# Kernel optimization log

Hardware: AMD Instinct MI355X
Metric: run time of the kernel (lower is better)

Reference implementation:

```python
import jax, jax.numpy as jnp
import numpy as np

N = 50000
E = 800000
D = 64


def sage_conv(x, src, dst, Wl, Wr, b, n_nodes):
    # message = x[src]; mean-aggregate by dst; then lin_l(mean) + lin_r(x) + b
    msg = x[src]                                             # [E, D] gather
    ssum = jax.ops.segment_sum(msg, dst, num_segments=n_nodes)  # [N, D]
    cnt = jax.ops.segment_sum(jnp.ones((msg.shape[0],), dtype=x.dtype), dst,
                              num_segments=n_nodes)          # [N]
    mean = ssum / jnp.maximum(cnt, 1.0)[:, None]             # scatter-mean (empty rows -> 0)
    return mean @ Wl.T + x @ Wr.T + b


def setup_inputs() -> dict:
    key = jax.random.key(0)
    ks = jax.random.split(key, 8)
    scale = 1.0 / np.sqrt(D)
    x = jax.random.normal(ks[0], (N, D), dtype=jnp.float32)
    edge_index = jax.random.randint(ks[1], (2, E), 0, N, dtype=jnp.int64)
    Wl1 = jax.random.normal(ks[2], (D, D), dtype=jnp.float32) * scale
    Wr1 = jax.random.normal(ks[3], (D, D), dtype=jnp.float32) * scale
    b1 = jnp.zeros((D,), dtype=jnp.float32)
    Wl2 = jax.random.normal(ks[4], (D, D), dtype=jnp.float32) * scale
    Wr2 = jax.random.normal(ks[5], (D, D), dtype=jnp.float32) * scale
    b2 = jnp.zeros((D,), dtype=jnp.float32)
    return {"x": x, "edge_index": edge_index, "Wl1": Wl1, "Wr1": Wr1, "b1": b1,
            "Wl2": Wl2, "Wr2": Wr2, "b2": b2}


def reference(x, edge_index, Wl1, Wr1, b1, Wl2, Wr2, b2):
    src, dst = edge_index[0], edge_index[1]
    n = x.shape[0]
    h = sage_conv(x, src, dst, Wl1, Wr1, b1, n)
    h = jax.nn.relu(h)
    out = sage_conv(h, src, dst, Wl2, Wr2, b2, n)
    return out
```

## Files before the change

### kernel.cpp

```cpp
#include <hip/hip_runtime.h>

#define D 64
#define CAP 64
#define LPAD 132
#define NPART 8

__global__ void fill_kernel(const int* __restrict__ src, const int* __restrict__ dst,
                            int* __restrict__ cnti, int* __restrict__ eidx,
                            int E, int N) {
    int part = blockIdx.x & (NPART - 1);
    int bip  = blockIdx.x >> 3;
    int span = (N + NPART - 1) / NPART;
    int lo = part * span;
    int hi = lo + span; if (hi > N) hi = N;
    int i = bip * blockDim.x + threadIdx.x;
    int stride = (gridDim.x >> 3) * blockDim.x;
    for (; i < E; i += stride) {
        int t = dst[i];
        if (t >= lo && t < hi) {
            int pos = atomicAdd(&cnti[t], 1);
            if (pos < CAP) eidx[(size_t)t * CAP + pos] = src[i];
        }
    }
}

__device__ __forceinline__ float dot4acc(float4 a, float4 w, float c) {
    c = fmaf(a.x, w.x, c);
    c = fmaf(a.y, w.y, c);
    c = fmaf(a.z, w.z, c);
    c = fmaf(a.w, w.w, c);
    return c;
}

__global__ __launch_bounds__(256, 2) void fused_kernel(
                             const float* __restrict__ xin,
                             const int* __restrict__ eidx,
                             const int* __restrict__ cnti,
                             const float* __restrict__ Wl,
                             const float* __restrict__ Wr,
                             const float* __restrict__ bias,
                             float* __restrict__ out,
                             int do_relu, int N) {
    __shared__ float ain[64][LPAD];
    __shared__ float wsh[64][LPAD];
    __shared__ float bsh[64];
    int tid = threadIdx.x;
    int nb = blockIdx.x * 64;

    for (int c = tid; c < 64 * 32; c += 256) {
        int d = c >> 5, kc = c & 31;
        float4 v;
        if (kc < 16) v = *reinterpret_cast<const float4*>(Wl + d * D + kc * 4);
        else         v = *reinterpret_cast<const float4*>(Wr + d * D + (kc - 16) * 4);
        *reinterpret_cast<float4*>(&wsh[d][kc * 4]) = v;
    }
    if (tid < 64) bsh[tid] = bias[tid];

    int g = tid >> 4;
    int lane = tid & 15;
    for (int ni = 0; ni < 4; ++ni) {
        int ln = ni * 16 + g;
        int node = nb + ln; if (node >= N) node = N - 1;
        int deg = cnti[node];
        int lim = deg > CAP ? CAP : deg;
        int last = lim - 1;
        const int* ep = eidx + (size_t)node * CAP;
        float4 acc = make_float4(0.f, 0.f, 0.f, 0.f);
        for (int i = 0; i < lim; i += 8) {
            int j1 = i + 1 > last ? last : i + 1;
            int j2 = i + 2 > last ? last : i + 2;
            int j3 = i + 3 > last ? last : i + 3;
            int j4 = i + 4 > last ? last : i + 4;
            int j5 = i + 5 > last ? last : i + 5;
            int j6 = i + 6 > last ? last : i + 6;
            int j7 = i + 7 > last ? last : i + 7;
            int e0 = ep[i];  int e1 = ep[j1]; int e2 = ep[j2]; int e3 = ep[j3];
            int e4 = ep[j4]; int e5 = ep[j5]; int e6 = ep[j6]; int e7 = ep[j7];
            float4 v0 = *reinterpret_cast<const float4*>(xin + (size_t)e0 * D + lane * 4);
            float4 v1 = *reinterpret_cast<const float4*>(xin + (size_t)e1 * D + lane * 4);
            float4 v2 = *reinterpret_cast<const float4*>(xin + (size_t)e2 * D + lane * 4);
            float4 v3 = *reinterpret_cast<const float4*>(xin + (size_t)e3 * D + lane * 4);
            float4 v4 = *reinterpret_cast<const float4*>(xin + (size_t)e4 * D + lane * 4);
            float4 v5 = *reinterpret_cast<const float4*>(xin + (size_t)e5 * D + lane * 4);
            float4 v6 = *reinterpret_cast<const float4*>(xin + (size_t)e6 * D + lane * 4);
            float4 v7 = *reinterpret_cast<const float4*>(xin + (size_t)e7 * D + lane * 4);
            float m1 = (i + 1 <= last) ? 1.f : 0.f;
            float m2 = (i + 2 <= last) ? 1.f : 0.f;
            float m3 = (i + 3 <= last) ? 1.f : 0.f;
            float m4 = (i + 4 <= last) ? 1.f : 0.f;
            float m5 = (i + 5 <= last) ? 1.f : 0.f;
            float m6 = (i + 6 <= last) ? 1.f : 0.f;
            float m7 = (i + 7 <= last) ? 1.f : 0.f;
            acc.x += v0.x; acc.y += v0.y; acc.z += v0.z; acc.w += v0.w;
            acc.x = fmaf(v1.x, m1, acc.x); acc.y = fmaf(v1.y, m1, acc.y);
            acc.z = fmaf(v1.z, m1, acc.z); acc.w = fmaf(v1.w, m1, acc.w);
            acc.x = fmaf(v2.x, m2, acc.x); acc.y = fmaf(v2.y, m2, acc.y);
            acc.z = fmaf(v2.z, m2, acc.z); acc.w = fmaf(v2.w, m2, acc.w);
            acc.x = fmaf(v3.x, m3, acc.x); acc.y = fmaf(v3.y, m3, acc.y);
            acc.z = fmaf(v3.z, m3, acc.z); acc.w = fmaf(v3.w, m3, acc.w);
            acc.x = fmaf(v4.x, m4, acc.x); acc.y = fmaf(v4.y, m4, acc.y);
            acc.z = fmaf(v4.z, m4, acc.z); acc.w = fmaf(v4.w, m4, acc.w);
            acc.x = fmaf(v5.x, m5, acc.x); acc.y = fmaf(v5.y, m5, acc.y);
            acc.z = fmaf(v5.z, m5, acc.z); acc.w = fmaf(v5.w, m5, acc.w);
            acc.x = fmaf(v6.x, m6, acc.x); acc.y = fmaf(v6.y, m6, acc.y);
            acc.z = fmaf(v6.z, m6, acc.z); acc.w = fmaf(v6.w, m6, acc.w);
            acc.x = fmaf(v7.x, m7, acc.x); acc.y = fmaf(v7.y, m7, acc.y);
            acc.z = fmaf(v7.z, m7, acc.z); acc.w = fmaf(v7.w, m7, acc.w);
        }
        float r = 1.0f / fmaxf((float)deg, 1.0f);
        acc.x *= r; acc.y *= r; acc.z *= r; acc.w *= r;
        *reinterpret_cast<float4*>(&ain[ln][lane * 4]) = acc;
        float4 xv = *reinterpret_cast<const float4*>(xin + (size_t)node * D + lane * 4);
        *reinterpret_cast<float4*>(&ain[ln][64 + lane * 4]) = xv;
    }
    __syncthreads();

    int tx = tid & 15;
    int ty = tid >> 4;

    float4 acc0 = make_float4(0.f, 0.f, 0.f, 0.f);
    float4 acc1 = make_float4(0.f, 0.f, 0.f, 0.f);
    float4 acc2 = make_float4(0.f, 0.f, 0.f, 0.f);
    float4 acc3 = make_float4(0.f, 0.f, 0.f, 0.f);

#pragma unroll 2
    for (int kc = 0; kc < 32; ++kc) {
        float4 a0 = *reinterpret_cast<const float4*>(&ain[ty +  0][kc * 4]);
        float4 a1 = *reinterpret_cast<const float4*>(&ain[ty + 16][kc * 4]);
        float4 a2 = *reinterpret_cast<const float4*>(&ain[ty + 32][kc * 4]);
        float4 a3 = *reinterpret_cast<const float4*>(&ain[ty + 48][kc * 4]);
        float4 w0 = *reinterpret_cast<const float4*>(&wsh[tx +  0][kc * 4]);
        float4 w1 = *reinterpret_cast<const float4*>(&wsh[tx + 16][kc * 4]);
        float4 w2 = *reinterpret_cast<const float4*>(&wsh[tx + 32][kc * 4]);
        float4 w3 = *reinterpret_cast<const float4*>(&wsh[tx + 48][kc * 4]);
        acc0.x = dot4acc(a0, w0, acc0.x); acc0.y = dot4acc(a0, w1, acc0.y);
        acc0.z = dot4acc(a0, w2, acc0.z); acc0.w = dot4acc(a0, w3, acc0.w);
        acc1.x = dot4acc(a1, w0, acc1.x); acc1.y = dot4acc(a1, w1, acc1.y);
        acc1.z = dot4acc(a1, w2, acc1.z); acc1.w = dot4acc(a1, w3, acc1.w);
        acc2.x = dot4acc(a2, w0, acc2.x); acc2.y = dot4acc(a2, w1, acc2.y);
        acc2.z = dot4acc(a2, w2, acc2.z); acc2.w = dot4acc(a2, w3, acc2.w);
        acc3.x = dot4acc(a3, w0, acc3.x); acc3.y = dot4acc(a3, w1, acc3.y);
        acc3.z = dot4acc(a3, w2, acc3.z); acc3.w = dot4acc(a3, w3, acc3.w);
    }

    float b0 = bsh[tx], b1 = bsh[tx + 16], b2 = bsh[tx + 32], b3 = bsh[tx + 48];
#define STORE_ROW(ACCV, I)                                                    \
    {                                                                         \
        int node = nb + ty + 16 * (I);                                        \
        if (node < N) {                                                       \
            float v0 = ACCV.x + b0, v1 = ACCV.y + b1,                         \
                  v2 = ACCV.z + b2, v3 = ACCV.w + b3;                         \
            if (do_relu) {                                                    \
                v0 = fmaxf(v0, 0.f); v1 = fmaxf(v1, 0.f);                     \
                v2 = fmaxf(v2, 0.f); v3 = fmaxf(v3, 0.f);                     \
            }                                                                 \
            float* op = out + (size_t)node * D;                               \
            op[tx] = v0; op[tx + 16] = v1; op[tx + 32] = v2; op[tx + 48] = v3;\
        }                                                                     \
    }
    STORE_ROW(acc0, 0)
    STORE_ROW(acc1, 1)
    STORE_ROW(acc2, 2)
    STORE_ROW(acc3, 3)
#undef STORE_ROW
}

extern "C" void kernel_launch(void* const* d_in, const int* in_sizes, int n_in,
                              void* d_out, int out_size, void* d_ws, size_t ws_size,
                              hipStream_t stream) {
    const float* x   = (const float*)d_in[0];
    const int*   ei  = (const int*)d_in[1];
    const float* Wl1 = (const float*)d_in[2];
    const float* Wr1 = (const float*)d_in[3];
    const float* b1  = (const float*)d_in[4];
    const float* Wl2 = (const float*)d_in[5];
    const float* Wr2 = (const float*)d_in[6];
    const float* b2  = (const float*)d_in[7];

    int N_ = in_sizes[0] / D;
    int E_ = in_sizes[1] / 2;
    const int* src = ei;
    const int* dst = ei + E_;

    int*   cnti = (int*)d_ws;
    int*   eidx = cnti + N_;
    float* h    = (float*)(eidx + (size_t)N_ * CAP);
    float* outp = (float*)d_out;

    hipMemsetAsync(cnti, 0, (size_t)N_ * sizeof(int), stream);
    fill_kernel<<<2048, 256, 0, stream>>>(src, dst, cnti, eidx, E_, N_);

    int blocks = (N_ + 63) / 64;
    fused_kernel<<<blocks, 256, 0, stream>>>(x, eidx, cnti, Wl1, Wr1, b1, h, 1, N_);
    fused_kernel<<<blocks, 256, 0, stream>>>(h, eidx, cnti, Wl2, Wr2, b2, outp, 0, N_);
}
```

Baseline: 219.4 us.

## Gather neighbor features from bf16 copies and store weights as bf16 in LDS

Adds a conversion kernel that writes a bf16 copy of x, and makes layer 1 also emit a bf16 copy of h. The neighbor gather in the fused kernel now reads 8 bytes per lane instead of 16, which halves the random-access gather traffic. Weights are packed as bf16 in LDS so the kernel uses less shared memory, and launch bounds are raised to 3 blocks per SM. The cost is an extra conversion pass, extra bf16 stores, and reduced precision in the aggregation and weights, which may break a tight tolerance.

```diff
diff --git a/kernel.cpp b/kernel.cpp
--- a/kernel.cpp
+++ b/kernel.cpp
@@ -3,7 +3,28 @@
 #define D 64
 #define CAP 64
 #define LPAD 132
+#define WPAD 136
 #define NPART 8
+
+__device__ __forceinline__ unsigned int f2bf(float f) {
+    unsigned int u = __float_as_uint(f);
+    return (u + 0x7fffu + ((u >> 16) & 1u)) >> 16;
+}
+__device__ __forceinline__ float bflo(unsigned int u) { return __uint_as_float(u << 16); }
+__device__ __forceinline__ float bfhi(unsigned int u) { return __uint_as_float(u & 0xffff0000u); }
+
+__global__ void convert_kernel(const float* __restrict__ in,
+                               unsigned short* __restrict__ outh, int total4) {
+    int i = blockIdx.x * blockDim.x + threadIdx.x;
+    int stride = gridDim.x * blockDim.x;
+    for (; i < total4; i += stride) {
+        float4 v = *reinterpret_cast<const float4*>(in + (size_t)i * 4);
+        uint2 p;
+        p.x = f2bf(v.x) | (f2bf(v.y) << 16);
+        p.y = f2bf(v.z) | (f2bf(v.w) << 16);
+        *reinterpret_cast<uint2*>(outh + (size_t)i * 4) = p;
+    }
+}
 
 __global__ void fill_kernel(const int* __restrict__ src, const int* __restrict__ dst,
                             int* __restrict__ cnti, int* __restrict__ eidx,
@@ -32,17 +53,19 @@
     return c;
 }
 
-__global__ __launch_bounds__(256, 2) void fused_kernel(
+__global__ __launch_bounds__(256, 3) void fused_kernel(
                              const float* __restrict__ xin,
+                             const unsigned short* __restrict__ gath,
                              const int* __restrict__ eidx,
                              const int* __restrict__ cnti,
                              const float* __restrict__ Wl,
                              const float* __restrict__ Wr,
                              const float* __restrict__ bias,
                              float* __restrict__ out,
+                             unsigned short* __restrict__ outh,
                              int do_relu, int N) {
     __shared__ float ain[64][LPAD];
-    __shared__ float wsh[64][LPAD];
+    __shared__ unsigned short wsh[64][WPAD];
     __shared__ float bsh[64];
     int tid = threadIdx.x;
     int nb = blockIdx.x * 64;
@@ -52,7 +75,10 @@
         float4 v;
         if (kc < 16) v = *reinterpret_cast<const float4*>(Wl + d * D + kc * 4);
         else         v = *reinterpret_cast<const float4*>(Wr + d * D + (kc - 16) * 4);
-        *reinterpret_cast<float4*>(&wsh[d][kc * 4]) = v;
+        uint2 p;
+        p.x = f2bf(v.x) | (f2bf(v.y) << 16);
+        p.y = f2bf(v.z) | (f2bf(v.w) << 16);
+        *reinterpret_cast<uint2*>(&wsh[d][kc * 4]) = p;
     }
     if (tid < 64) bsh[tid] = bias[tid];
 
@@ -76,14 +102,14 @@
             int j7 = i + 7 > last ? last : i + 7;
             int e0 = ep[i];  int e1 = ep[j1]; int e2 = ep[j2]; int e3 = ep[j3];
             int e4 = ep[j4]; int e5 = ep[j5]; int e6 = ep[j6]; int e7 = ep[j7];
-            float4 v0 = *reinterpret_cast<const float4*>(xin + (size_t)e0 * D + lane * 4);
-            float4 v1 = *reinterpret_cast<const float4*>(xin + (size_t)e1 * D + lane * 4);
-            float4 v2 = *reinterpret_cast<const float4*>(xin + (size_t)e2 * D + lane * 4);
-            float4 v3 = *reinterpret_cast<const float4*>(xin + (size_t)e3 * D + lane * 4);
-            float4 v4 = *reinterpret_cast<const float4*>(xin + (size_t)e4 * D + lane * 4);
-            float4 v5 = *reinterpret_cast<const float4*>(xin + (size_t)e5 * D + lane * 4);
-            float4 v6 = *reinterpret_cast<const float4*>(xin + (size_t)e6 * D + lane * 4);
-            float4 v7 = *reinterpret_cast<const float4*>(xin + (size_t)e7 * D + lane * 4);
+            uint2 w0 = *reinterpret_cast<const uint2*>(gath + (size_t)e0 * D + lane * 4);
+            uint2 w1 = *reinterpret_cast<const uint2*>(gath + (size_t)e1 * D + lane * 4);
+            uint2 w2 = *reinterpret_cast<const uint2*>(gath + (size_t)e2 * D + lane * 4);
+            uint2 w3 = *reinterpret_cast<const uint2*>(gath + (size_t)e3 * D + lane * 4);
+            uint2 w4 = *reinterpret_cast<const uint2*>(gath + (size_t)e4 * D + lane * 4);
+            uint2 w5 = *reinterpret_cast<const uint2*>(gath + (size_t)e5 * D + lane * 4);
+            uint2 w6 = *reinterpret_cast<const uint2*>(gath + (size_t)e6 * D + lane * 4);
+            uint2 w7 = *reinterpret_cast<const uint2*>(gath + (size_t)e7 * D + lane * 4);
             float m1 = (i + 1 <= last) ? 1.f : 0.f;
             float m2 = (i + 2 <= last) ? 1.f : 0.f;
             float m3 = (i + 3 <= last) ? 1.f : 0.f;
@@ -91,21 +117,22 @@
             float m5 = (i + 5 <= last) ? 1.f : 0.f;
             float m6 = (i + 6 <= last) ? 1.f : 0.f;
             float m7 = (i + 7 <= last) ? 1.f : 0.f;
-            acc.x += v0.x; acc.y += v0.y; acc.z += v0.z; acc.w += v0.w;
-            acc.x = fmaf(v1.x, m1, acc.x); acc.y = fmaf(v1.y, m1, acc.y);
-            acc.z = fmaf(v1.z, m1, acc.z); acc.w = fmaf(v1.w, m1, acc.w);
-            acc.x = fmaf(v2.x, m2, acc.x); acc.y = fmaf(v2.y, m2, acc.y);
-            acc.z = fmaf(v2.z, m2, acc.z); acc.w = fmaf(v2.w, m2, acc.w);
-            acc.x = fmaf(v3.x, m3, acc.x); acc.y = fmaf(v3.y, m3, acc.y);
-            acc.z = fmaf(v3.z, m3, acc.z); acc.w = fmaf(v3.w, m3, acc.w);
-            acc.x = fmaf(v4.x, m4, acc.x); acc.y = fmaf(v4.y, m4, acc.y);
-            acc.z = fmaf(v4.z, m4, acc.z); acc.w = fmaf(v4.w, m4, acc.w);
-            acc.x = fmaf(v5.x, m5, acc.x); acc.y = fmaf(v5.y, m5, acc.y);
-            acc.z = fmaf(v5.z, m5, acc.z); acc.w = fmaf(v5.w, m5, acc.w);
-            acc.x = fmaf(v6.x, m6, acc.x); acc.y = fmaf(v6.y, m6, acc.y);
-            acc.z = fmaf(v6.z, m6, acc.z); acc.w = fmaf(v6.w, m6, acc.w);
-            acc.x = fmaf(v7.x, m7, acc.x); acc.y = fmaf(v7.y, m7, acc.y);
-            acc.z = fmaf(v7.z, m7, acc.z); acc.w = fmaf(v7.w, m7, acc.w);
+            acc.x += bflo(w0.x); acc.y += bfhi(w0.x);
+            acc.z += bflo(w0.y); acc.w += bfhi(w0.y);
+            acc.x = fmaf(bflo(w1.x), m1, acc.x); acc.y = fmaf(bfhi(w1.x), m1, acc.y);
+            acc.z = fmaf(bflo(w1.y), m1, acc.z); acc.w = fmaf(bfhi(w1.y), m1, acc.w);
+            acc.x = fmaf(bflo(w2.x), m2, acc.x); acc.y = fmaf(bfhi(w2.x), m2, acc.y);
+            acc.z = fmaf(bflo(w2.y), m2, acc.z); acc.w = fmaf(bfhi(w2.y), m2, acc.w);
+            acc.x = fmaf(bflo(w3.x), m3, acc.x); acc.y = fmaf(bfhi(w3.x), m3, acc.y);
+            acc.z = fmaf(bflo(w3.y), m3, acc.z); acc.w = fmaf(bfhi(w3.y), m3, acc.w);
+            acc.x = fmaf(bflo(w4.x), m4, acc.x); acc.y = fmaf(bfhi(w4.x), m4, acc.y);
+            acc.z = fmaf(bflo(w4.y), m4, acc.z); acc.w = fmaf(bfhi(w4.y), m4, acc.w);
+            acc.x = fmaf(bflo(w5.x), m5, acc.x); acc.y = fmaf(bfhi(w5.x), m5, acc.y);
+            acc.z = fmaf(bflo(w5.y), m5, acc.z); acc.w = fmaf(bfhi(w5.y), m5, acc.w);
+            acc.x = fmaf(bflo(w6.x), m6, acc.x); acc.y = fmaf(bfhi(w6.x), m6, acc.y);
+            acc.z = fmaf(bflo(w6.y), m6, acc.z); acc.w = fmaf(bfhi(w6.y), m6, acc.w);
+            acc.x = fmaf(bflo(w7.x), m7, acc.x); acc.y = fmaf(bfhi(w7.x), m7, acc.y);
+            acc.z = fmaf(bflo(w7.y), m7, acc.z); acc.w = fmaf(bfhi(w7.y), m7, acc.w);
         }
         float r = 1.0f / fmaxf((float)deg, 1.0f);
         acc.x *= r; acc.y *= r; acc.z *= r; acc.w *= r;
@@ -129,10 +156,14 @@
         float4 a1 = *reinterpret_cast<const float4*>(&ain[ty + 16][kc * 4]);
         float4 a2 = *reinterpret_cast<const float4*>(&ain[ty + 32][kc * 4]);
         float4 a3 = *reinterpret_cast<const float4*>(&ain[ty + 48][kc * 4]);
-        float4 w0 = *reinterpret_cast<const float4*>(&wsh[tx +  0][kc * 4]);
-        float4 w1 = *reinterpret_cast<const float4*>(&wsh[tx + 16][kc * 4]);
-        float4 w2 = *reinterpret_cast<const float4*>(&wsh[tx + 32][kc * 4]);
-        float4 w3 = *reinterpret_cast<const float4*>(&wsh[tx + 48][kc * 4]);
+        uint2 q0 = *reinterpret_cast<const uint2*>(&wsh[tx +  0][kc * 4]);
+        uint2 q1 = *reinterpret_cast<const uint2*>(&wsh[tx + 16][kc * 4]);
+        uint2 q2 = *reinterpret_cast<const uint2*>(&wsh[tx + 32][kc * 4]);
+        uint2 q3 = *reinterpret_cast<const uint2*>(&wsh[tx + 48][kc * 4]);
+        float4 w0 = make_float4(bflo(q0.x), bfhi(q0.x), bflo(q0.y), bfhi(q0.y));
+        float4 w1 = make_float4(bflo(q1.x), bfhi(q1.x), bflo(q1.y), bfhi(q1.y));
+        float4 w2 = make_float4(bflo(q2.x), bfhi(q2.x), bflo(q2.y), bfhi(q2.y));
+        float4 w3 = make_float4(bflo(q3.x), bfhi(q3.x), bflo(q3.y), bfhi(q3.y));
         acc0.x = dot4acc(a0, w0, acc0.x); acc0.y = dot4acc(a0, w1, acc0.y);
         acc0.z = dot4acc(a0, w2, acc0.z); acc0.w = dot4acc(a0, w3, acc0.w);
         acc1.x = dot4acc(a1, w0, acc1.x); acc1.y = dot4acc(a1, w1, acc1.y);
@@ -156,6 +187,13 @@
             }                                                                 \
             float* op = out + (size_t)node * D;                               \
             op[tx] = v0; op[tx + 16] = v1; op[tx + 32] = v2; op[tx + 48] = v3;\
+            if (outh) {                                                       \
+                unsigned short* oh = outh + (size_t)node * D;                 \
+                oh[tx]      = (unsigned short)f2bf(v0);                       \
+                oh[tx + 16] = (unsigned short)f2bf(v1);                       \
+                oh[tx + 32] = (unsigned short)f2bf(v2);                       \
+                oh[tx + 48] = (unsigned short)f2bf(v3);                       \
+            }                                                                 \
         }                                                                     \
     }
     STORE_ROW(acc0, 0)
@@ -182,15 +220,19 @@
     const int* src = ei;
     const int* dst = ei + E_;
 
-    int*   cnti = (int*)d_ws;
-    int*   eidx = cnti + N_;
-    float* h    = (float*)(eidx + (size_t)N_ * CAP);
+    int*            cnti = (int*)d_ws;
+    int*            eidx = cnti + N_;
+    float*          h    = (float*)(eidx + (size_t)N_ * CAP);
+    unsigned short* xh   = (unsigned short*)(h + (size_t)N_ * D);
+    unsigned short* hh   = xh + (size_t)N_ * D;
     float* outp = (float*)d_out;
 
     hipMemsetAsync(cnti, 0, (size_t)N_ * sizeof(int), stream);
+    convert_kernel<<<2048, 256, 0, stream>>>(x, xh, N_ * D / 4);
     fill_kernel<<<2048, 256, 0, stream>>>(src, dst, cnti, eidx, E_, N_);
 
     int blocks = (N_ + 63) / 64;
-    fused_kernel<<<blocks, 256, 0, stream>>>(x, eidx, cnti, Wl1, Wr1, b1, h, 1, N_);
-    fused_kernel<<<blocks, 256, 0, stream>>>(h, eidx, cnti, Wl2, Wr2, b2, outp, 0, N_);
-}
+    fused_kernel<<<blocks, 256, 0, stream>>>(x, xh, eidx, cnti, Wl1, Wr1, b1, h, hh, 1, N_);
+    fused_kernel<<<blocks, 256, 0, stream>>>(h, hh, eidx, cnti, Wl2, Wr2, b2, outp,
+                                             (unsigned short*)nullptr, 0, N_);
+}
```

Result: no change. 221.6 us (+1.0%).
